# Kernel tuning notes

Hardware: AMD Instinct MI355X
Metric: run time of the kernel (lower is better)

## Reference

```python
import jax, jax.numpy as jnp
import numpy as np

ALPHA = 0.01  # LeakyReLU negative slope
D_OUT = 128   # output_size; a1 is split at this index


def setup_inputs() -> dict:
    key = jax.random.key(0)
    k1, k2, k3, k4 = jax.random.split(key, 4)
    B, N, M, D_IN = 8, 2048, 2048, 256
    input_tensor1 = jax.random.normal(k1, (B, N, D_IN), dtype=jnp.float32)
    input_tensor2 = jax.random.normal(k2, (B, M, D_IN), dtype=jnp.float32)
    attention_mask2 = jnp.zeros((B, 1, M), dtype=jnp.float32)
    # Parameters (xavier-uniform-like scaled normals are fine for a numeric reference)
    W1 = jax.random.normal(k3, (D_IN, D_OUT), dtype=jnp.float32) * (1.414 * np.sqrt(2.0 / (D_IN + D_OUT)))
    a1 = jax.random.normal(k4, (2 * D_OUT, 1), dtype=jnp.float32) * (1.414 * np.sqrt(2.0 / (2 * D_OUT + 1)))
    return {"input_tensor1": input_tensor1, "input_tensor2": input_tensor2,
            "attention_mask2": attention_mask2, "W1": W1, "a1": a1}


def reference(input_tensor1, input_tensor2, attention_mask2, W1, a1):
    # Projections (dropout is identity in eval / p=0)
    Wh1 = jnp.einsum('bnd,de->bne', input_tensor1, W1)  # (B, N, E)
    Wh2 = jnp.einsum('bmd,de->bme', input_tensor2, W1)  # (B, M, E)
    # GAT-style additive score: broadcast outer-sum of two rank-1 projections
    att1 = jnp.einsum('bne,eo->bno', Wh1, a1[:D_OUT, :])   # (B, N, 1)
    att2 = jnp.einsum('bme,eo->bmo', Wh2, a1[D_OUT:, :])   # (B, M, 1)
    e = att1 + jnp.swapaxes(att2, 1, 2)                     # (B, N, M)
    e = jnp.where(e > 0, e, ALPHA * e)                      # LeakyReLU
    scores = e + attention_mask2                            # additive mask
    probs = jax.nn.softmax(scores, axis=-1)                 # (B, N, M)
    context = jnp.einsum('bnm,bme->bne', probs, Wh2)        # (B, N, E)
    return (context, probs)
```

## Files before the change

kernel.cpp:

```cpp
#include <hip/hip_runtime.h>

#define B 8
#define N 2048
#define M 2048
#define DIN 256
#define E 128
#define ALPHA 0.01f

typedef __attribute__((ext_vector_type(8))) short bf16x8;
typedef __attribute__((ext_vector_type(4))) float f32x4;

__device__ inline ushort f2bf(float x) {
  unsigned u = __float_as_uint(x);
  u = (u + 0x7FFFu + ((u >> 16) & 1u)) >> 16;
  return (ushort)u;
}

__device__ inline float leaky_mask(float a1r, float a2, float mk) {
  float s = a1r + a2;
  s = s > 0.f ? s : ALPHA * s;
  return s + mk;
}

__global__ __launch_bounds__(256) void prep_v_kernel(
    const float* __restrict__ W1, const float* __restrict__ a1,
    float* __restrict__ v1, float* __restrict__ v2) {
  int k = threadIdx.x;
  float s1 = 0.f, s2 = 0.f;
#pragma unroll 8
  for (int e = 0; e < E; ++e) {
    float w = W1[k * E + e];
    s1 += w * a1[e];
    s2 += w * a1[E + e];
  }
  v1[k] = s1;
  v2[k] = s2;
}

__global__ __launch_bounds__(256) void att_kernel(
    const float* __restrict__ in1, const float* __restrict__ in2,
    const float* __restrict__ v1, const float* __restrict__ v2,
    float* __restrict__ att1, float* __restrict__ att2) {
  int wave = blockIdx.x * 4 + (threadIdx.x >> 6);
  int lane = threadIdx.x & 63;
  const float* src;
  const float* v;
  float* dst;
  int row;
  if (wave < B * N) {
    src = in1; v = v1; dst = att1; row = wave;
  } else {
    src = in2; v = v2; dst = att2; row = wave - B * N;
  }
  float4 x = *(const float4*)(src + (size_t)row * DIN + lane * 4);
  float4 vv = *(const float4*)(v + lane * 4);
  float d = x.x * vv.x + x.y * vv.y + x.z * vv.z + x.w * vv.w;
#pragma unroll
  for (int off = 32; off; off >>= 1) d += __shfl_down(d, off, 64);
  if (lane == 0) dst[row] = d;
}

__global__ __launch_bounds__(256) void wh2_kernel(
    const float* __restrict__ in2, const float* __restrict__ W1,
    ushort* __restrict__ Wb) {
  __shared__ float a[32][DIN];
  int r0 = blockIdx.x * 32;
#pragma unroll
  for (int i = 0; i < 8; ++i) {
    int f = (threadIdx.x + i * 256) * 4;
    int r = f >> 8, k = f & 255;
    *(float4*)&a[r][k] = *(const float4*)(in2 + (size_t)(r0 + r) * DIN + k);
  }
  __syncthreads();
  int c  = (threadIdx.x & 31) * 4;
  int tr = (threadIdx.x >> 5) * 4;
  float acc[4][4] = {};
  for (int k = 0; k < DIN; ++k) {
    float4 b = *(const float4*)(W1 + k * E + c);
#pragma unroll
    for (int r = 0; r < 4; ++r) {
      float av = a[tr + r][k];
      acc[r][0] += av * b.x;
      acc[r][1] += av * b.y;
      acc[r][2] += av * b.z;
      acc[r][3] += av * b.w;
    }
  }
#pragma unroll
  for (int r = 0; r < 4; ++r) {
    int m = r0 + tr + r;
    size_t gbase = (size_t)(m >> 3) * 128 * 8 + (m & 7);
#pragma unroll
    for (int j = 0; j < 4; ++j)
      Wb[gbase + (size_t)(c + j) * 8] = f2bf(acc[r][j]);
  }
}

__global__ __launch_bounds__(256) void stats_kernel(
    const float* __restrict__ att1, const float* __restrict__ att2,
    const float* __restrict__ mask,
    float* __restrict__ rowmax, float* __restrict__ rowinv) {
  int row = blockIdx.x * 4 + (threadIdx.x >> 6);
  int lane = threadIdx.x & 63;
  int b = row >> 11;
  float a1r = att1[row];
  const float* a2 = att2 + b * M;
  const float* mk = mask + b * M;
  float mx = -1e30f;
#pragma unroll
  for (int i = 0; i < 8; ++i) {
    int m = (lane + i * 64) * 4;
    float4 av = *(const float4*)(a2 + m);
    float4 mv = *(const float4*)(mk + m);
    mx = fmaxf(mx, leaky_mask(a1r, av.x, mv.x));
    mx = fmaxf(mx, leaky_mask(a1r, av.y, mv.y));
    mx = fmaxf(mx, leaky_mask(a1r, av.z, mv.z));
    mx = fmaxf(mx, leaky_mask(a1r, av.w, mv.w));
  }
#pragma unroll
  for (int off = 32; off; off >>= 1) mx = fmaxf(mx, __shfl_xor(mx, off, 64));
  float sum = 0.f;
#pragma unroll
  for (int i = 0; i < 8; ++i) {
    int m = (lane + i * 64) * 4;
    float4 av = *(const float4*)(a2 + m);
    float4 mv = *(const float4*)(mk + m);
    sum += __expf(leaky_mask(a1r, av.x, mv.x) - mx);
    sum += __expf(leaky_mask(a1r, av.y, mv.y) - mx);
    sum += __expf(leaky_mask(a1r, av.z, mv.z) - mx);
    sum += __expf(leaky_mask(a1r, av.w, mv.w) - mx);
  }
#pragma unroll
  for (int off = 32; off; off >>= 1) sum += __shfl_xor(sum, off, 64);
  if (lane == 0) {
    rowmax[row] = mx;
    rowinv[row] = 1.f / sum;
  }
}

__global__ __launch_bounds__(256) void fused_kernel(
    const float* __restrict__ att1, const float* __restrict__ att2,
    const float* __restrict__ mask, const float* __restrict__ rowmax,
    const float* __restrict__ rowinv, const ushort* __restrict__ Wb,
    float* __restrict__ probs, float* __restrict__ ctx) {
  __shared__ float att2s[M];
  __shared__ float masks[M];
  __shared__ ushort ldsB[2 * 8 * 128 * 8];

  int rt = blockIdx.x & 63;
  int b  = blockIdx.x >> 6;
  int row0 = b * N + rt * 32;
  int t = threadIdx.x;
  int lane = t & 63;
  int w = t >> 6;
  int quad = lane >> 4;
  int l16 = lane & 15;
  int m0w = (w & 1) * 16;
  int h   = w >> 1;

#pragma unroll
  for (int i = 0; i < 2; ++i) {
    int idx = (t + i * 256) * 4;
    *(float4*)&att2s[idx] = *(const float4*)(att2 + b * M + idx);
    *(float4*)&masks[idx] = *(const float4*)(mask + b * M + idx);
  }

  int myrow = row0 + m0w + l16;
  float a1v  = att1[myrow];
  float rmxL = rowmax[myrow];
  float rinL = rowinv[myrow];
  float* prow = probs + (size_t)myrow * M;

  f32x4 acc[8] = {};

  for (int k0 = 0; k0 < M; k0 += 128) {
    {
      const char* g =
          (const char*)(Wb + ((size_t)b * 256 + (k0 >> 3)) * 1024);
      char* l = (char*)ldsB;
      int base = w * 1024 + lane * 16;
#pragma unroll
      for (int i = 0; i < 8; ++i) {
        int off = base + i * 4096;
        __builtin_amdgcn_global_load_lds(
            (const __attribute__((address_space(1))) void*)(g + off),
            (__attribute__((address_space(3))) void*)(l + off), 16, 0, 0);
      }
    }
    __syncthreads();
    int kc = k0 + h * 64;
#pragma unroll
    for (int ks = 0; ks < 64; ks += 32) {
      int kb = kc + ks + quad * 8;
      float4 a0 = *(const float4*)&att2s[kb];
      float4 a1q = *(const float4*)&att2s[kb + 4];
      float4 k0v = *(const float4*)&masks[kb];
      float4 k1v = *(const float4*)&masks[kb + 4];
      float p[8];
      p[0] = __expf(leaky_mask(a1v, a0.x, k0v.x) - rmxL) * rinL;
      p[1] = __expf(leaky_mask(a1v, a0.y, k0v.y) - rmxL) * rinL;
      p[2] = __expf(leaky_mask(a1v, a0.z, k0v.z) - rmxL) * rinL;
      p[3] = __expf(leaky_mask(a1v, a0.w, k0v.w) - rmxL) * rinL;
      p[4] = __expf(leaky_mask(a1v, a1q.x, k1v.x) - rmxL) * rinL;
      p[5] = __expf(leaky_mask(a1v, a1q.y, k1v.y) - rmxL) * rinL;
      p[6] = __expf(leaky_mask(a1v, a1q.z, k1v.z) - rmxL) * rinL;
      p[7] = __expf(leaky_mask(a1v, a1q.w, k1v.w) - rmxL) * rinL;
      bf16x8 af;
#pragma unroll
      for (int j = 0; j < 8; ++j) af[j] = (short)f2bf(p[j]);
      *(float4*)(prow + kb)     = make_float4(p[0], p[1], p[2], p[3]);
      *(float4*)(prow + kb + 4) = make_float4(p[4], p[5], p[6], p[7]);
      int gl = h * 8 + (ks >> 3) + quad;
#pragma unroll
      for (int cf = 0; cf < 8; ++cf) {
        int n = cf * 16 + l16;
        bf16x8 bfb = *(const bf16x8*)&ldsB[((size_t)gl * 128 + n) * 8];
        acc[cf] =
            __builtin_amdgcn_mfma_f32_16x16x32_bf16(af, bfb, acc[cf], 0, 0, 0);
      }
    }
    __syncthreads();
  }

  float* red = (float*)ldsB;
  if (h == 1) {
    int base = ((w & 1) * 64 + lane) * 36;
#pragma unroll
    for (int cf = 0; cf < 8; ++cf)
      *(f32x4*)&red[base + cf * 4] = acc[cf];
  }
  __syncthreads();
  if (h == 0) {
    int base = ((w & 1) * 64 + lane) * 36;
#pragma unroll
    for (int cf = 0; cf < 8; ++cf) {
      f32x4 o = *(const f32x4*)&red[base + cf * 4];
      int nn = cf * 16 + l16;
#pragma unroll
      for (int reg = 0; reg < 4; ++reg) {
        int rr = row0 + m0w + quad * 4 + reg;
        ctx[(size_t)rr * E + nn] = acc[cf][reg] + o[reg];
      }
    }
  }
}

extern "C" void kernel_launch(void* const* d_in, const int* in_sizes, int n_in,
                              void* d_out, int out_size, void* d_ws,
                              size_t ws_size, hipStream_t stream) {
  (void)in_sizes; (void)n_in; (void)out_size; (void)ws_size;
  const float* in1  = (const float*)d_in[0];
  const float* in2  = (const float*)d_in[1];
  const float* mask = (const float*)d_in[2];
  const float* W1   = (const float*)d_in[3];
  const float* a1   = (const float*)d_in[4];

  float* ws     = (float*)d_ws;
  float* v1     = ws;
  float* v2     = v1 + DIN;
  float* att1   = v2 + DIN;
  float* att2   = att1 + B * N;
  float* rowmax = att2 + B * M;
  float* rowinv = rowmax + B * N;
  ushort* Wb    = (ushort*)(rowinv + B * N);

  float* ctx   = (float*)d_out;
  float* probs = ctx + (size_t)B * N * E;

  hipLaunchKernelGGL(prep_v_kernel, dim3(1), dim3(256), 0, stream, W1, a1, v1, v2);
  hipLaunchKernelGGL(att_kernel, dim3((B * N + B * M) / 4), dim3(256), 0, stream,
                     in1, in2, v1, v2, att1, att2);
  hipLaunchKernelGGL(wh2_kernel, dim3(B * M / 32), dim3(256), 0, stream,
                     in2, W1, Wb);
  hipLaunchKernelGGL(stats_kernel, dim3(B * N / 4), dim3(256), 0, stream,
                     att1, att2, mask, rowmax, rowinv);
  hipLaunchKernelGGL(fused_kernel, dim3(B * N / 32), dim3(256), 0, stream,
                     att1, att2, mask, rowmax, rowinv, Wb, probs, ctx);
}
```

Measured before the change: 230.9 us.

## Fuse attention scores and row stats into main kernel with double-buffered B loads

Removes the separate att_kernel and stats_kernel. att2 is now computed from the fp32 Wh2 accumulators inside wh2_kernel, and att1 plus the per-row max and log-sum are computed at the start of fused_kernel from LDS-staged att2 and mask. The main loop switches to exp2 with a folded log-normalizer and packed bf16 conversion. It also uses nontemporal stores for probs, double-buffered async global-to-LDS loads of Wb with a single barrier per step, and a block-index swizzle. In exchange, each block recomputes row stats redundantly, and att2 is now derived from unrounded fp32 Wh2 values.

```diff
diff --git a/kernel.cpp b/kernel.cpp
--- a/kernel.cpp
+++ b/kernel.cpp
@@ -6,9 +6,16 @@
 #define DIN 256
 #define E 128
 #define ALPHA 0.01f
+#define LOG2E 1.44269504088896340736f
 
 typedef __attribute__((ext_vector_type(8))) short bf16x8;
 typedef __attribute__((ext_vector_type(4))) float f32x4;
+
+#if __has_builtin(__builtin_amdgcn_exp2f)
+#define EXP2(x) __builtin_amdgcn_exp2f(x)
+#else
+#define EXP2(x) exp2f(x)
+#endif
 
 __device__ inline ushort f2bf(float x) {
   unsigned u = __float_as_uint(x);
@@ -16,53 +23,31 @@
   return (ushort)u;
 }
 
-__device__ inline float leaky_mask(float a1r, float a2, float mk) {
-  float s = a1r + a2;
-  s = s > 0.f ? s : ALPHA * s;
-  return s + mk;
-}
+__device__ inline float lrelu(float s) { return fmaxf(s, ALPHA * s); }
+
+__device__ inline float getc(const float4& v, int i) {
+  return i == 0 ? v.x : i == 1 ? v.y : i == 2 ? v.z : v.w;
+}
+
+#define GLDS(gp, lp)                                          \
+  __builtin_amdgcn_global_load_lds(                           \
+      (const __attribute__((address_space(1))) void*)(gp),    \
+      (__attribute__((address_space(3))) void*)(lp), 16, 0, 0)
 
 __global__ __launch_bounds__(256) void prep_v_kernel(
     const float* __restrict__ W1, const float* __restrict__ a1,
-    float* __restrict__ v1, float* __restrict__ v2) {
+    float* __restrict__ v1) {
   int k = threadIdx.x;
-  float s1 = 0.f, s2 = 0.f;
+  float s1 = 0.f;
 #pragma unroll 8
-  for (int e = 0; e < E; ++e) {
-    float w = W1[k * E + e];
-    s1 += w * a1[e];
-    s2 += w * a1[E + e];
-  }
+  for (int e = 0; e < E; ++e) s1 += W1[k * E + e] * a1[e];
   v1[k] = s1;
-  v2[k] = s2;
-}
-
-__global__ __launch_bounds__(256) void att_kernel(
-    const float* __restrict__ in1, const float* __restrict__ in2,
-    const float* __restrict__ v1, const float* __restrict__ v2,
-    float* __restrict__ att1, float* __restrict__ att2) {
-  int wave = blockIdx.x * 4 + (threadIdx.x >> 6);
-  int lane = threadIdx.x & 63;
-  const float* src;
-  const float* v;
-  float* dst;
-  int row;
-  if (wave < B * N) {
-    src = in1; v = v1; dst = att1; row = wave;
-  } else {
-    src = in2; v = v2; dst = att2; row = wave - B * N;
-  }
-  float4 x = *(const float4*)(src + (size_t)row * DIN + lane * 4);
-  float4 vv = *(const float4*)(v + lane * 4);
-  float d = x.x * vv.x + x.y * vv.y + x.z * vv.z + x.w * vv.w;
-#pragma unroll
-  for (int off = 32; off; off >>= 1) d += __shfl_down(d, off, 64);
-  if (lane == 0) dst[row] = d;
 }
 
 __global__ __launch_bounds__(256) void wh2_kernel(
     const float* __restrict__ in2, const float* __restrict__ W1,
-    ushort* __restrict__ Wb) {
+    const float* __restrict__ a1, ushort* __restrict__ Wb,
+    float* __restrict__ att2) {
   __shared__ float a[32][DIN];
   int r0 = blockIdx.x * 32;
 #pragma unroll
@@ -75,159 +60,203 @@
   int c  = (threadIdx.x & 31) * 4;
   int tr = (threadIdx.x >> 5) * 4;
   float acc[4][4] = {};
-  for (int k = 0; k < DIN; ++k) {
-    float4 b = *(const float4*)(W1 + k * E + c);
-#pragma unroll
-    for (int r = 0; r < 4; ++r) {
-      float av = a[tr + r][k];
-      acc[r][0] += av * b.x;
-      acc[r][1] += av * b.y;
-      acc[r][2] += av * b.z;
-      acc[r][3] += av * b.w;
+  for (int k4 = 0; k4 < DIN; k4 += 4) {
+    float4 av0 = *(const float4*)&a[tr + 0][k4];
+    float4 av1 = *(const float4*)&a[tr + 1][k4];
+    float4 av2 = *(const float4*)&a[tr + 2][k4];
+    float4 av3 = *(const float4*)&a[tr + 3][k4];
+#pragma unroll
+    for (int kk = 0; kk < 4; ++kk) {
+      float4 bv = *(const float4*)(W1 + (size_t)(k4 + kk) * E + c);
+      float x0 = getc(av0, kk), x1 = getc(av1, kk);
+      float x2 = getc(av2, kk), x3 = getc(av3, kk);
+      acc[0][0] += x0 * bv.x; acc[0][1] += x0 * bv.y;
+      acc[0][2] += x0 * bv.z; acc[0][3] += x0 * bv.w;
+      acc[1][0] += x1 * bv.x; acc[1][1] += x1 * bv.y;
+      acc[1][2] += x1 * bv.z; acc[1][3] += x1 * bv.w;
+      acc[2][0] += x2 * bv.x; acc[2][1] += x2 * bv.y;
+      acc[2][2] += x2 * bv.z; acc[2][3] += x2 * bv.w;
+      acc[3][0] += x3 * bv.x; acc[3][1] += x3 * bv.y;
+      acc[3][2] += x3 * bv.z; acc[3][3] += x3 * bv.w;
     }
   }
 #pragma unroll
   for (int r = 0; r < 4; ++r) {
     int m = r0 + tr + r;
-    size_t gbase = (size_t)(m >> 3) * 128 * 8 + (m & 7);
+    size_t gbase = (size_t)(m >> 3) * 1024 + (m & 7);
 #pragma unroll
     for (int j = 0; j < 4; ++j)
       Wb[gbase + (size_t)(c + j) * 8] = f2bf(acc[r][j]);
   }
-}
-
-__global__ __launch_bounds__(256) void stats_kernel(
-    const float* __restrict__ att1, const float* __restrict__ att2,
-    const float* __restrict__ mask,
-    float* __restrict__ rowmax, float* __restrict__ rowinv) {
-  int row = blockIdx.x * 4 + (threadIdx.x >> 6);
-  int lane = threadIdx.x & 63;
-  int b = row >> 11;
-  float a1r = att1[row];
-  const float* a2 = att2 + b * M;
-  const float* mk = mask + b * M;
-  float mx = -1e30f;
-#pragma unroll
-  for (int i = 0; i < 8; ++i) {
-    int m = (lane + i * 64) * 4;
-    float4 av = *(const float4*)(a2 + m);
-    float4 mv = *(const float4*)(mk + m);
-    mx = fmaxf(mx, leaky_mask(a1r, av.x, mv.x));
-    mx = fmaxf(mx, leaky_mask(a1r, av.y, mv.y));
-    mx = fmaxf(mx, leaky_mask(a1r, av.z, mv.z));
-    mx = fmaxf(mx, leaky_mask(a1r, av.w, mv.w));
-  }
-#pragma unroll
-  for (int off = 32; off; off >>= 1) mx = fmaxf(mx, __shfl_xor(mx, off, 64));
-  float sum = 0.f;
-#pragma unroll
-  for (int i = 0; i < 8; ++i) {
-    int m = (lane + i * 64) * 4;
-    float4 av = *(const float4*)(a2 + m);
-    float4 mv = *(const float4*)(mk + m);
-    sum += __expf(leaky_mask(a1r, av.x, mv.x) - mx);
-    sum += __expf(leaky_mask(a1r, av.y, mv.y) - mx);
-    sum += __expf(leaky_mask(a1r, av.z, mv.z) - mx);
-    sum += __expf(leaky_mask(a1r, av.w, mv.w) - mx);
-  }
-#pragma unroll
-  for (int off = 32; off; off >>= 1) sum += __shfl_xor(sum, off, 64);
-  if (lane == 0) {
-    rowmax[row] = mx;
-    rowinv[row] = 1.f / sum;
+  float4 a1b = *(const float4*)(a1 + E + c);
+  float p0 = acc[0][0]*a1b.x + acc[0][1]*a1b.y + acc[0][2]*a1b.z + acc[0][3]*a1b.w;
+  float p1 = acc[1][0]*a1b.x + acc[1][1]*a1b.y + acc[1][2]*a1b.z + acc[1][3]*a1b.w;
+  float p2 = acc[2][0]*a1b.x + acc[2][1]*a1b.y + acc[2][2]*a1b.z + acc[2][3]*a1b.w;
+  float p3 = acc[3][0]*a1b.x + acc[3][1]*a1b.y + acc[3][2]*a1b.z + acc[3][3]*a1b.w;
+#pragma unroll
+  for (int off = 16; off; off >>= 1) {
+    p0 += __shfl_xor(p0, off, 32);
+    p1 += __shfl_xor(p1, off, 32);
+    p2 += __shfl_xor(p2, off, 32);
+    p3 += __shfl_xor(p3, off, 32);
+  }
+  if ((threadIdx.x & 31) == 0) {
+    att2[r0 + tr + 0] = p0;
+    att2[r0 + tr + 1] = p1;
+    att2[r0 + tr + 2] = p2;
+    att2[r0 + tr + 3] = p3;
   }
 }
 
 __global__ __launch_bounds__(256) void fused_kernel(
-    const float* __restrict__ att1, const float* __restrict__ att2,
-    const float* __restrict__ mask, const float* __restrict__ rowmax,
-    const float* __restrict__ rowinv, const ushort* __restrict__ Wb,
-    float* __restrict__ probs, float* __restrict__ ctx) {
-  __shared__ float att2s[M];
-  __shared__ float masks[M];
-  __shared__ ushort ldsB[2 * 8 * 128 * 8];
-
-  int rt = blockIdx.x & 63;
-  int b  = blockIdx.x >> 6;
+    const float* __restrict__ in1, const float* __restrict__ v1,
+    const float* __restrict__ att2, const float* __restrict__ mask,
+    const ushort* __restrict__ Wb, float* __restrict__ probs,
+    float* __restrict__ ctx) {
+  __shared__ __align__(16) char smem[49408];
+  float* att2s = (float*)smem;
+  float* masks = (float*)(smem + 8192);
+  char* bufs   = smem + 16384;
+  float* rowC  = (float*)(smem + 49152);
+  float* rowA  = (float*)(smem + 49280);
+
+  int wg = (blockIdx.x & 7) * 64 + (blockIdx.x >> 3);
+  int rt = wg & 63;
+  int b  = wg >> 6;
   int row0 = b * N + rt * 32;
-  int t = threadIdx.x;
-  int lane = t & 63;
-  int w = t >> 6;
-  int quad = lane >> 4;
-  int l16 = lane & 15;
+  int t0 = threadIdx.x;
+
+  const char* gW = (const char*)(Wb + (size_t)b * M * E);
+
+#define STAGE(bsel, tt)                                        \
+  do {                                                         \
+    const char* _g = gW + (size_t)(tt) * 16384 + t0 * 16;      \
+    char* _l = bufs + (bsel) * 16384 + t0 * 16;                \
+    GLDS(_g, _l);                                              \
+    GLDS(_g + 4096, _l + 4096);                                \
+    GLDS(_g + 8192, _l + 8192);                                \
+    GLDS(_g + 12288, _l + 12288);                              \
+  } while (0)
+
+  {
+    const char* gA = (const char*)(att2 + (size_t)b * M);
+    const char* gK = (const char*)(mask + (size_t)b * M);
+    char* lA = (char*)att2s;
+    char* lK = (char*)masks;
+    int so = t0 * 16;
+    GLDS(gA + so, lA + so);
+    GLDS(gA + so + 4096, lA + so + 4096);
+    GLDS(gK + so, lK + so);
+    GLDS(gK + so + 4096, lK + so + 4096);
+    STAGE(0, 0);
+    STAGE(1, 1);
+  }
+  __syncthreads();
+
+  {
+    int srow = t0 >> 3, sub = t0 & 7;
+    const float4* x4 = (const float4*)(in1 + (size_t)(row0 + srow) * DIN);
+    const float4* v4 = (const float4*)v1;
+    float d = 0.f;
+#pragma unroll
+    for (int i = 0; i < 8; ++i) {
+      float4 x = x4[sub + i * 8], vv = v4[sub + i * 8];
+      d += x.x * vv.x + x.y * vv.y + x.z * vv.z + x.w * vv.w;
+    }
+    d += __shfl_xor(d, 1, 8);
+    d += __shfl_xor(d, 2, 8);
+    d += __shfl_xor(d, 4, 8);
+    float sa1 = d;
+    const float4* a4 = (const float4*)att2s;
+    const float4* k4 = (const float4*)masks;
+    float mx = -3.0e38f;
+#pragma unroll 4
+    for (int i = 0; i < 64; ++i) {
+      int idx = sub + i * 8;
+      float4 a = a4[idx], k = k4[idx];
+      float s0 = lrelu(sa1 + a.x) + k.x;
+      float s1 = lrelu(sa1 + a.y) + k.y;
+      float s2 = lrelu(sa1 + a.z) + k.z;
+      float s3 = lrelu(sa1 + a.w) + k.w;
+      mx = fmaxf(mx, fmaxf(fmaxf(s0, s1), fmaxf(s2, s3)));
+    }
+    mx = fmaxf(mx, __shfl_xor(mx, 1, 8));
+    mx = fmaxf(mx, __shfl_xor(mx, 2, 8));
+    mx = fmaxf(mx, __shfl_xor(mx, 4, 8));
+    float cm = -mx * LOG2E;
+    float sum = 0.f;
+#pragma unroll 4
+    for (int i = 0; i < 64; ++i) {
+      int idx = sub + i * 8;
+      float4 a = a4[idx], k = k4[idx];
+      sum += EXP2(fmaf(lrelu(sa1 + a.x) + k.x, LOG2E, cm));
+      sum += EXP2(fmaf(lrelu(sa1 + a.y) + k.y, LOG2E, cm));
+      sum += EXP2(fmaf(lrelu(sa1 + a.z) + k.z, LOG2E, cm));
+      sum += EXP2(fmaf(lrelu(sa1 + a.w) + k.w, LOG2E, cm));
+    }
+    sum += __shfl_xor(sum, 1, 8);
+    sum += __shfl_xor(sum, 2, 8);
+    sum += __shfl_xor(sum, 4, 8);
+    if (sub == 0) {
+      rowC[srow] = cm - __log2f(sum);
+      rowA[srow] = sa1;
+    }
+  }
+  __syncthreads();
+
+  int lane = t0 & 63, w = t0 >> 6;
+  int quad = lane >> 4, l16 = lane & 15;
   int m0w = (w & 1) * 16;
   int h   = w >> 1;
-
-#pragma unroll
-  for (int i = 0; i < 2; ++i) {
-    int idx = (t + i * 256) * 4;
-    *(float4*)&att2s[idx] = *(const float4*)(att2 + b * M + idx);
-    *(float4*)&masks[idx] = *(const float4*)(mask + b * M + idx);
-  }
-
   int myrow = row0 + m0w + l16;
-  float a1v  = att1[myrow];
-  float rmxL = rowmax[myrow];
-  float rinL = rowinv[myrow];
+  float a1v  = rowA[m0w + l16];
+  float crow = rowC[m0w + l16];
   float* prow = probs + (size_t)myrow * M;
 
   f32x4 acc[8] = {};
 
-  for (int k0 = 0; k0 < M; k0 += 128) {
-    {
-      const char* g =
-          (const char*)(Wb + ((size_t)b * 256 + (k0 >> 3)) * 1024);
-      char* l = (char*)ldsB;
-      int base = w * 1024 + lane * 16;
-#pragma unroll
-      for (int i = 0; i < 8; ++i) {
-        int off = base + i * 4096;
-        __builtin_amdgcn_global_load_lds(
-            (const __attribute__((address_space(1))) void*)(g + off),
-            (__attribute__((address_space(3))) void*)(l + off), 16, 0, 0);
-      }
-    }
-    __syncthreads();
-    int kc = k0 + h * 64;
-#pragma unroll
-    for (int ks = 0; ks < 64; ks += 32) {
-      int kb = kc + ks + quad * 8;
-      float4 a0 = *(const float4*)&att2s[kb];
-      float4 a1q = *(const float4*)&att2s[kb + 4];
-      float4 k0v = *(const float4*)&masks[kb];
-      float4 k1v = *(const float4*)&masks[kb + 4];
-      float p[8];
-      p[0] = __expf(leaky_mask(a1v, a0.x, k0v.x) - rmxL) * rinL;
-      p[1] = __expf(leaky_mask(a1v, a0.y, k0v.y) - rmxL) * rinL;
-      p[2] = __expf(leaky_mask(a1v, a0.z, k0v.z) - rmxL) * rinL;
-      p[3] = __expf(leaky_mask(a1v, a0.w, k0v.w) - rmxL) * rinL;
-      p[4] = __expf(leaky_mask(a1v, a1q.x, k1v.x) - rmxL) * rinL;
-      p[5] = __expf(leaky_mask(a1v, a1q.y, k1v.y) - rmxL) * rinL;
-      p[6] = __expf(leaky_mask(a1v, a1q.z, k1v.z) - rmxL) * rinL;
-      p[7] = __expf(leaky_mask(a1v, a1q.w, k1v.w) - rmxL) * rinL;
-      bf16x8 af;
-#pragma unroll
-      for (int j = 0; j < 8; ++j) af[j] = (short)f2bf(p[j]);
-      *(float4*)(prow + kb)     = make_float4(p[0], p[1], p[2], p[3]);
-      *(float4*)(prow + kb + 4) = make_float4(p[4], p[5], p[6], p[7]);
-      int gl = h * 8 + (ks >> 3) + quad;
-#pragma unroll
-      for (int cf = 0; cf < 8; ++cf) {
-        int n = cf * 16 + l16;
-        bf16x8 bfb = *(const bf16x8*)&ldsB[((size_t)gl * 128 + n) * 8];
-        acc[cf] =
-            __builtin_amdgcn_mfma_f32_16x16x32_bf16(af, bfb, acc[cf], 0, 0, 0);
-      }
-    }
-    __syncthreads();
-  }
-
-  float* red = (float*)ldsB;
+  for (int t = 0; t < 32; ++t) {
+    const ushort* bw = (const ushort*)(bufs + (t & 1) * 16384);
+    int kb = t * 64 + h * 32 + quad * 8;
+    float4 a0  = *(const float4*)&att2s[kb];
+    float4 a1q = *(const float4*)&att2s[kb + 4];
+    float4 k0  = *(const float4*)&masks[kb];
+    float4 k1  = *(const float4*)&masks[kb + 4];
+    float p0 = EXP2(fmaf(lrelu(a1v + a0.x)  + k0.x, LOG2E, crow));
+    float p1 = EXP2(fmaf(lrelu(a1v + a0.y)  + k0.y, LOG2E, crow));
+    float p2 = EXP2(fmaf(lrelu(a1v + a0.z)  + k0.z, LOG2E, crow));
+    float p3 = EXP2(fmaf(lrelu(a1v + a0.w)  + k0.w, LOG2E, crow));
+    float p4 = EXP2(fmaf(lrelu(a1v + a1q.x) + k1.x, LOG2E, crow));
+    float p5 = EXP2(fmaf(lrelu(a1v + a1q.y) + k1.y, LOG2E, crow));
+    float p6 = EXP2(fmaf(lrelu(a1v + a1q.z) + k1.z, LOG2E, crow));
+    float p7 = EXP2(fmaf(lrelu(a1v + a1q.w) + k1.w, LOG2E, crow));
+    union { unsigned u[4]; bf16x8 v; } af;
+    asm("v_cvt_pk_bf16_f32 %0, %1, %2" : "=v"(af.u[0]) : "v"(p0), "v"(p1));
+    asm("v_cvt_pk_bf16_f32 %0, %1, %2" : "=v"(af.u[1]) : "v"(p2), "v"(p3));
+    asm("v_cvt_pk_bf16_f32 %0, %1, %2" : "=v"(af.u[2]) : "v"(p4), "v"(p5));
+    asm("v_cvt_pk_bf16_f32 %0, %1, %2" : "=v"(af.u[3]) : "v"(p6), "v"(p7));
+    f32x4 st0 = {p0, p1, p2, p3};
+    f32x4 st1 = {p4, p5, p6, p7};
+    __builtin_nontemporal_store(st0, (f32x4*)(prow + kb));
+    __builtin_nontemporal_store(st1, (f32x4*)(prow + kb + 4));
+    const ushort* bb = bw + (size_t)((h * 4 + quad) * 128) * 8;
+#pragma unroll
+    for (int cf = 0; cf < 8; ++cf) {
+      bf16x8 bfb = *(const bf16x8*)(bb + (size_t)(cf * 16 + l16) * 8);
+      acc[cf] =
+          __builtin_amdgcn_mfma_f32_16x16x32_bf16(af.v, bfb, acc[cf], 0, 0, 0);
+    }
+    asm volatile("s_waitcnt vmcnt(2) lgkmcnt(0)" ::: "memory");
+    __builtin_amdgcn_s_barrier();
+    if (t < 30) STAGE(t & 1, t + 2);
+  }
+#undef STAGE
+
+  float* red = (float*)bufs;
   if (h == 1) {
     int base = ((w & 1) * 64 + lane) * 36;
 #pragma unroll
-    for (int cf = 0; cf < 8; ++cf)
-      *(f32x4*)&red[base + cf * 4] = acc[cf];
+    for (int cf = 0; cf < 8; ++cf) *(f32x4*)&red[base + cf * 4] = acc[cf];
   }
   __syncthreads();
   if (h == 0) {
@@ -255,25 +284,17 @@
   const float* W1   = (const float*)d_in[3];
   const float* a1   = (const float*)d_in[4];
 
-  float* ws     = (float*)d_ws;
-  float* v1     = ws;
-  float* v2     = v1 + DIN;
-  float* att1   = v2 + DIN;
-  float* att2   = att1 + B * N;
-  float* rowmax = att2 + B * M;
-  float* rowinv = rowmax + B * N;
-  ushort* Wb    = (ushort*)(rowinv + B * N);
+  float* ws   = (float*)d_ws;
+  float* v1   = ws;
+  float* att2 = v1 + DIN;
+  ushort* Wb  = (ushort*)(att2 + B * M);
 
   float* ctx   = (float*)d_out;
   float* probs = ctx + (size_t)B * N * E;
 
-  hipLaunchKernelGGL(prep_v_kernel, dim3(1), dim3(256), 0, stream, W1, a1, v1, v2);
-  hipLaunchKernelGGL(att_kernel, dim3((B * N + B * M) / 4), dim3(256), 0, stream,
-                     in1, in2, v1, v2, att1, att2);
+  hipLaunchKernelGGL(prep_v_kernel, dim3(1), dim3(256), 0, stream, W1, a1, v1);
   hipLaunchKernelGGL(wh2_kernel, dim3(B * M / 32), dim3(256), 0, stream,
-                     in2, W1, Wb);
-  hipLaunchKernelGGL(stats_kernel, dim3(B * N / 4), dim3(256), 0, stream,
-                     att1, att2, mask, rowmax, rowinv);
+                     in2, W1, a1, Wb, att2);
   hipLaunchKernelGGL(fused_kernel, dim3(B * N / 32), dim3(256), 0, stream,
-                     att1, att2, mask, rowmax, rowinv, Wb, probs, ctx);
-}
+                     in1, v1, att2, mask, Wb, probs, ctx);
+}
```

Measured after the change: 226.2 us. -2.1%, faster.
